# Optimization experiments

Measured on AMD Instinct MI355X. Metric: run time of the kernel, lower is better.

## Reference

```python
import jax, jax.numpy as jnp
import numpy as np

S = 7          # grid size
B = 2          # boxes per cell
C = 20         # classes
STEP = 1.0 / S
L_COORD = 5.0
L_NOOBJ = 0.5
EPS = 1e-6


def setup_inputs() -> dict:
    key = jax.random.key(0)
    k1, k2, k3 = jax.random.split(key, 3)
    N = 16384
    pred = jax.random.normal(k1, (N, S, S, B * 5 + C), dtype=jnp.float32)
    target = jax.random.uniform(k2, (N, S, S, B * 5 + C), dtype=jnp.float32)
    objm = jax.random.uniform(k3, (N, S, S, B)) < 0.05
    tb = target[..., :10].reshape(N, S, S, B, 5)
    tb = tb.at[..., 4].set(tb[..., 4] * objm)
    target = target.at[..., :10].set(tb.reshape(N, S, S, 10))
    return {"pred": pred, "target": target}


def _convert_box(box, gx, gy):
    # box: [N,S,S,B,4] in cell-relative (x,y) + image-relative (w,h)
    # gx: grid x index (axis 2), gy: grid y index (axis 1); matches conver_box
    x = (box[..., 0] + gx) * STEP - box[..., 2] * 0.5
    y = (box[..., 1] + gy) * STEP - box[..., 3] * 0.5
    out = jnp.stack([x, y, box[..., 2], box[..., 3]], axis=-1)
    return jnp.clip(out, 0.0, 1.0)


def _iou(b1, b2):
    x1, y1, w1, h1 = b1[..., 0], b1[..., 1], b1[..., 2], b1[..., 3]
    x2, y2, w2, h2 = b2[..., 0], b2[..., 1], b2[..., 2], b2[..., 3]
    inter_w = jnp.maximum(w1 + w2 - (jnp.maximum(x1 + w1, x2 + w2) - jnp.minimum(x1, x2)), 0.0)
    inter_h = jnp.maximum(h1 + h2 - (jnp.maximum(y1 + h1, y2 + h2) - jnp.minimum(y1, y2)), 0.0)
    inter = inter_w * inter_h
    union = w1 * h1 + w2 * h2 - inter + EPS
    return inter / union


def reference(pred, target):
    N = pred.shape[0]
    pb = pred[..., :10].reshape(N, S, S, B, 5)   # [N,S,S,B,5]
    tb = target[..., :10].reshape(N, S, S, B, 5)
    pc = pred[..., 10:]                           # [N,S,S,C]
    tc = target[..., 10:]
    obj0 = tb[..., 4] > 0                         # [N,S,S,B]
    sig = jnp.any(obj0, axis=-1)                  # [N,S,S]
    # grid indices: torch loop uses (y=dim1, x=dim2), conver_box index=[x, y]
    gx = jnp.arange(S, dtype=pred.dtype).reshape(1, 1, S, 1)
    gy = jnp.arange(S, dtype=pred.dtype).reshape(1, S, 1, 1)
    ious = _iou(_convert_box(pb[..., :4], gx, gy), _convert_box(tb[..., :4], gx, gy))  # [N,S,S,B]
    # responsible box = argmax IoU (first index on ties, matching torch .max(0))
    best = jnp.argmax(ious, axis=-1)[..., None] == jnp.arange(B)  # [N,S,S,B]
    obj = obj0 & best
    zero = jnp.zeros((), pred.dtype)
    # confidence losses
    dconf2 = (pb[..., 4] - tb[..., 4]) ** 2
    obj_loss = jnp.sum(jnp.where(obj, dconf2, zero))
    noobj_loss = jnp.sum(jnp.where(~obj, dconf2, zero))
    # coordinate losses
    obj_e = obj[..., None]
    dxy2 = (pb[..., :2] - tb[..., :2]) ** 2
    xy_loss = jnp.sum(jnp.where(obj_e, dxy2, zero))
    pwh = jnp.maximum(pb[..., 2:4], 0.0)
    dwh2 = (jnp.sqrt(tb[..., 2:4] + EPS) - jnp.sqrt(pwh + EPS)) ** 2
    wh_loss = jnp.sum(jnp.where(obj_e, dwh2, zero))
    # class loss over cells containing any object
    dcls2 = (pc - tc) ** 2
    class_loss = jnp.sum(jnp.where(sig[..., None], dcls2, zero))
    loss = obj_loss + L_NOOBJ * noobj_loss + L_COORD * xy_loss + L_COORD * wh_loss + class_loss
    return loss / N
```

## Files before the change

### kernel.cpp

```cpp
#include <hip/hip_runtime.h>

#define STEPV (1.0f / 7.0f)
#define L_COORD 5.0f
#define L_NOOBJ 0.5f
#define EPSV 1e-6f

#define TILE 128
#define FLOATS_PER_CELL 30
#define TILE_F4 (TILE * FLOATS_PER_CELL / 4)

typedef const __attribute__((address_space(1))) void cg_void;
typedef __attribute__((address_space(3))) void ls_void;

__global__ __launch_bounds__(384) void yolo_loss_kernel(
    const float* __restrict__ pred,
    const float* __restrict__ tgt,
    float* __restrict__ partials)
{
    __shared__ float4 bufP4[TILE_F4];
    __shared__ float4 bufT4[TILE_F4];

    const int tid  = threadIdx.x;
    const int w    = tid >> 6;
    const int lane = tid & 63;

    if (w < 3) {
        const float4* g = reinterpret_cast<const float4*>(pred)
                        + (size_t)blockIdx.x * TILE_F4 + w * 320 + lane;
        #pragma unroll
        for (int i = 0; i < 5; ++i)
            __builtin_amdgcn_global_load_lds((cg_void*)(g + i * 64),
                                             (ls_void*)(bufP4 + w * 320 + i * 64),
                                             16, 0, 0);
    } else {
        const float4* g = reinterpret_cast<const float4*>(tgt)
                        + (size_t)blockIdx.x * TILE_F4 + (w - 3) * 320 + lane;
        #pragma unroll
        for (int i = 0; i < 5; ++i)
            __builtin_amdgcn_global_load_lds((cg_void*)(g + i * 64),
                                             (ls_void*)(bufT4 + (w - 3) * 320 + i * 64),
                                             16, 0, 0);
    }
    __syncthreads();

    const float* bufP = reinterpret_cast<const float*>(bufP4);
    const float* bufT = reinterpret_cast<const float*>(bufT4);

    float loss = 0.0f;

    if (tid < TILE) {
        const int cid  = tid;
        const int cell = blockIdx.x * TILE + cid;
        const float* p = bufP + cid * FLOATS_PER_CELL;
        const float* t = bufT + cid * FLOATS_PER_CELL;
        float pv[10], tv[10];
        #pragma unroll
        for (int k = 0; k < 5; ++k) {
            float2 a = *reinterpret_cast<const float2*>(p + 2 * k);
            pv[2 * k] = a.x; pv[2 * k + 1] = a.y;
            float2 b = *reinterpret_cast<const float2*>(t + 2 * k);
            tv[2 * k] = b.x; tv[2 * k + 1] = b.y;
        }

        int ij = cell % 49;
        float gy = (float)(ij / 7);
        float gx = (float)(ij % 7);

        float iou[2];
        #pragma unroll
        for (int b = 0; b < 2; ++b) {
            const float* pb = pv + b * 5;
            const float* tb = tv + b * 5;
            float x1 = fminf(fmaxf((pb[0] + gx) * STEPV - pb[2] * 0.5f, 0.f), 1.f);
            float y1 = fminf(fmaxf((pb[1] + gy) * STEPV - pb[3] * 0.5f, 0.f), 1.f);
            float w1 = fminf(fmaxf(pb[2], 0.f), 1.f);
            float h1 = fminf(fmaxf(pb[3], 0.f), 1.f);
            float x2 = fminf(fmaxf((tb[0] + gx) * STEPV - tb[2] * 0.5f, 0.f), 1.f);
            float y2 = fminf(fmaxf((tb[1] + gy) * STEPV - tb[3] * 0.5f, 0.f), 1.f);
            float w2 = fminf(fmaxf(tb[2], 0.f), 1.f);
            float h2 = fminf(fmaxf(tb[3], 0.f), 1.f);
            float iw = fmaxf(w1 + w2 - (fmaxf(x1 + w1, x2 + w2) - fminf(x1, x2)), 0.f);
            float ih = fmaxf(h1 + h2 - (fmaxf(y1 + h1, y2 + h2) - fminf(y1, y2)), 0.f);
            float inter = iw * ih;
            float uni = w1 * h1 + w2 * h2 - inter + EPSV;
            iou[b] = inter / uni;
        }
        int best = (iou[1] > iou[0]) ? 1 : 0;

        float obj_l = 0.f, noobj_l = 0.f, xy_l = 0.f, wh_l = 0.f;
        #pragma unroll
        for (int b = 0; b < 2; ++b) {
            const float* pb = pv + b * 5;
            const float* tb = tv + b * 5;
            bool obj = (tb[4] > 0.f) && (b == best);
            float dc = pb[4] - tb[4];
            dc *= dc;
            if (obj) {
                obj_l += dc;
                float dx = pb[0] - tb[0];
                float dy = pb[1] - tb[1];
                xy_l += dx * dx + dy * dy;
                float sw = sqrtf(tb[2] + EPSV) - sqrtf(fmaxf(pb[2], 0.f) + EPSV);
                float sh = sqrtf(tb[3] + EPSV) - sqrtf(fmaxf(pb[3], 0.f) + EPSV);
                wh_l += sw * sw + sh * sh;
            } else {
                noobj_l += dc;
            }
        }
        loss = obj_l + L_NOOBJ * noobj_l + L_COORD * (xy_l + wh_l);
    } else {
        const int q   = tid - TILE;
        const int cid = q >> 1;
        const int sub = q & 1;
        const float* p = bufP + cid * FLOATS_PER_CELL + 10 + sub * 10;
        const float* t = bufT + cid * FLOATS_PER_CELL + 10 + sub * 10;
        float t4 = bufT[cid * FLOATS_PER_CELL + 4];
        float t9 = bufT[cid * FLOATS_PER_CELL + 9];
        bool sig = (t4 > 0.f) || (t9 > 0.f);

        float cls = 0.f;
        #pragma unroll
        for (int k = 0; k < 5; ++k) {
            float2 a = *reinterpret_cast<const float2*>(p + 2 * k);
            float2 b = *reinterpret_cast<const float2*>(t + 2 * k);
            float d0 = a.x - b.x;
            float d1 = a.y - b.y;
            cls += d0 * d0 + d1 * d1;
        }
        loss = sig ? cls : 0.0f;
    }

    #pragma unroll
    for (int off = 32; off > 0; off >>= 1)
        loss += __shfl_down(loss, off, 64);

    __shared__ float wsum[6];
    if (lane == 0) wsum[w] = loss;
    __syncthreads();
    if (tid == 0) {
        float s = 0.f;
        #pragma unroll
        for (int k = 0; k < 6; ++k) s += wsum[k];
        partials[blockIdx.x] = s;
    }
}

__global__ __launch_bounds__(1024) void yolo_finalize(
    const float* __restrict__ partials,
    float* __restrict__ out, int nparts, float invN)
{
    double s = 0.0;
    for (int i = threadIdx.x; i < nparts; i += 1024)
        s += (double)partials[i];

    #pragma unroll
    for (int off = 32; off > 0; off >>= 1)
        s += __shfl_down(s, off, 64);

    __shared__ double wsum[16];
    int lane = threadIdx.x & 63;
    int wid  = threadIdx.x >> 6;
    if (lane == 0) wsum[wid] = s;
    __syncthreads();
    if (threadIdx.x == 0) {
        double tot = 0.0;
        #pragma unroll
        for (int k = 0; k < 16; ++k) tot += wsum[k];
        out[0] = (float)(tot * (double)invN);
    }
}

extern "C" void kernel_launch(void* const* d_in, const int* in_sizes, int n_in,
                              void* d_out, int out_size, void* d_ws, size_t ws_size,
                              hipStream_t stream)
{
    const float* pred = (const float*)d_in[0];
    const float* tgt  = (const float*)d_in[1];
    float* out      = (float*)d_out;
    float* partials = (float*)d_ws;

    int ncells = in_sizes[0] / FLOATS_PER_CELL;
    int N = ncells / 49;
    int blocks = ncells / TILE;

    yolo_loss_kernel<<<blocks, 384, 0, stream>>>(pred, tgt, partials);
    yolo_finalize<<<1, 1024, 0, stream>>>(partials, out, blocks, 1.0f / (float)N);
}
```

Measured before the change: 36.22 us.

## Persistent grid with double-buffered async global-to-LDS tile prefetch

Replaces the one-tile-per-block launch with a fixed grid of 512 persistent blocks that stride over tiles. The next tile is prefetched into a second LDS buffer with global_load_lds while the current one is computed, using explicit vmcnt waits and barriers. The goal is to overlap memory latency with compute, cut block launch overhead, and shrink the finalize reduction to 512 partials. LDS per block doubles, which can lower occupancy, and the hand-written waitcnt ordering is fragile.

```diff
diff --git a/kernel.cpp b/kernel.cpp
--- a/kernel.cpp
+++ b/kernel.cpp
@@ -7,127 +7,147 @@
 
 #define TILE 128
 #define FLOATS_PER_CELL 30
-#define TILE_F4 (TILE * FLOATS_PER_CELL / 4)
+#define TILE_F4 960
+#define NBLK 512
+#define NTHREADS 384
 
 typedef const __attribute__((address_space(1))) void cg_void;
 typedef __attribute__((address_space(3))) void ls_void;
 
-__global__ __launch_bounds__(384) void yolo_loss_kernel(
+__global__ __launch_bounds__(NTHREADS) void yolo_loss_kernel(
     const float* __restrict__ pred,
     const float* __restrict__ tgt,
-    float* __restrict__ partials)
+    float* __restrict__ partials,
+    int ntiles)
 {
-    __shared__ float4 bufP4[TILE_F4];
-    __shared__ float4 bufT4[TILE_F4];
+    __shared__ float4 buf[2][2 * TILE_F4];
 
     const int tid  = threadIdx.x;
     const int w    = tid >> 6;
     const int lane = tid & 63;
 
-    if (w < 3) {
-        const float4* g = reinterpret_cast<const float4*>(pred)
-                        + (size_t)blockIdx.x * TILE_F4 + w * 320 + lane;
-        #pragma unroll
-        for (int i = 0; i < 5; ++i)
-            __builtin_amdgcn_global_load_lds((cg_void*)(g + i * 64),
-                                             (ls_void*)(bufP4 + w * 320 + i * 64),
-                                             16, 0, 0);
-    } else {
-        const float4* g = reinterpret_cast<const float4*>(tgt)
-                        + (size_t)blockIdx.x * TILE_F4 + (w - 3) * 320 + lane;
-        #pragma unroll
-        for (int i = 0; i < 5; ++i)
-            __builtin_amdgcn_global_load_lds((cg_void*)(g + i * 64),
-                                             (ls_void*)(bufT4 + (w - 3) * 320 + i * 64),
-                                             16, 0, 0);
-    }
-    __syncthreads();
-
-    const float* bufP = reinterpret_cast<const float*>(bufP4);
-    const float* bufT = reinterpret_cast<const float*>(bufT4);
+    const int wh   = (w < 3) ? w : (w - 3);
+    const int toff = (w < 3) ? 0 : TILE_F4;
+    const float4* gbase = reinterpret_cast<const float4*>(w < 3 ? pred : tgt);
+
+    #define STAGE(tile_, b_)                                                     \
+        do {                                                                     \
+            const float4* g_ = gbase + (size_t)(tile_) * TILE_F4 + wh * 320 + lane; \
+            float4* l_ = &buf[(b_)][toff + wh * 320];                            \
+            _Pragma("unroll")                                                    \
+            for (int i_ = 0; i_ < 5; ++i_)                                       \
+                __builtin_amdgcn_global_load_lds((cg_void*)(g_ + i_ * 64),       \
+                                                 (ls_void*)(l_ + i_ * 64),       \
+                                                 16, 0, 0);                      \
+        } while (0)
 
     float loss = 0.0f;
-
-    if (tid < TILE) {
-        const int cid  = tid;
-        const int cell = blockIdx.x * TILE + cid;
-        const float* p = bufP + cid * FLOATS_PER_CELL;
-        const float* t = bufT + cid * FLOATS_PER_CELL;
-        float pv[10], tv[10];
-        #pragma unroll
-        for (int k = 0; k < 5; ++k) {
-            float2 a = *reinterpret_cast<const float2*>(p + 2 * k);
-            pv[2 * k] = a.x; pv[2 * k + 1] = a.y;
-            float2 b = *reinterpret_cast<const float2*>(t + 2 * k);
-            tv[2 * k] = b.x; tv[2 * k + 1] = b.y;
+    int it = 0;
+
+    STAGE(blockIdx.x, 0);
+
+    for (int tile = blockIdx.x; tile < ntiles; tile += NBLK, ++it) {
+        const int b = it & 1;
+        const int nxt = tile + NBLK;
+
+        if (nxt < ntiles) {
+            STAGE(nxt, b ^ 1);
+            asm volatile("s_waitcnt vmcnt(5)" ::: "memory");
+        } else {
+            asm volatile("s_waitcnt vmcnt(0)" ::: "memory");
         }
-
-        int ij = cell % 49;
-        float gy = (float)(ij / 7);
-        float gx = (float)(ij % 7);
-
-        float iou[2];
-        #pragma unroll
-        for (int b = 0; b < 2; ++b) {
-            const float* pb = pv + b * 5;
-            const float* tb = tv + b * 5;
-            float x1 = fminf(fmaxf((pb[0] + gx) * STEPV - pb[2] * 0.5f, 0.f), 1.f);
-            float y1 = fminf(fmaxf((pb[1] + gy) * STEPV - pb[3] * 0.5f, 0.f), 1.f);
-            float w1 = fminf(fmaxf(pb[2], 0.f), 1.f);
-            float h1 = fminf(fmaxf(pb[3], 0.f), 1.f);
-            float x2 = fminf(fmaxf((tb[0] + gx) * STEPV - tb[2] * 0.5f, 0.f), 1.f);
-            float y2 = fminf(fmaxf((tb[1] + gy) * STEPV - tb[3] * 0.5f, 0.f), 1.f);
-            float w2 = fminf(fmaxf(tb[2], 0.f), 1.f);
-            float h2 = fminf(fmaxf(tb[3], 0.f), 1.f);
-            float iw = fmaxf(w1 + w2 - (fmaxf(x1 + w1, x2 + w2) - fminf(x1, x2)), 0.f);
-            float ih = fmaxf(h1 + h2 - (fmaxf(y1 + h1, y2 + h2) - fminf(y1, y2)), 0.f);
-            float inter = iw * ih;
-            float uni = w1 * h1 + w2 * h2 - inter + EPSV;
-            iou[b] = inter / uni;
+        __builtin_amdgcn_sched_barrier(0);
+        __builtin_amdgcn_s_barrier();
+        asm volatile("" ::: "memory");
+
+        const float* bufP = reinterpret_cast<const float*>(&buf[b][0]);
+        const float* bufT = reinterpret_cast<const float*>(&buf[b][TILE_F4]);
+
+        if (tid < TILE) {
+            const int cid  = tid;
+            const int cell = tile * TILE + cid;
+            const float* p = bufP + cid * FLOATS_PER_CELL;
+            const float* t = bufT + cid * FLOATS_PER_CELL;
+            float pv[10], tv[10];
+            #pragma unroll
+            for (int k = 0; k < 5; ++k) {
+                float2 a = *reinterpret_cast<const float2*>(p + 2 * k);
+                pv[2 * k] = a.x; pv[2 * k + 1] = a.y;
+                float2 c = *reinterpret_cast<const float2*>(t + 2 * k);
+                tv[2 * k] = c.x; tv[2 * k + 1] = c.y;
+            }
+
+            int ij = cell % 49;
+            float gy = (float)(ij / 7);
+            float gx = (float)(ij % 7);
+
+            float iou[2];
+            #pragma unroll
+            for (int bb = 0; bb < 2; ++bb) {
+                const float* pb = pv + bb * 5;
+                const float* tb = tv + bb * 5;
+                float x1 = fminf(fmaxf((pb[0] + gx) * STEPV - pb[2] * 0.5f, 0.f), 1.f);
+                float y1 = fminf(fmaxf((pb[1] + gy) * STEPV - pb[3] * 0.5f, 0.f), 1.f);
+                float w1 = fminf(fmaxf(pb[2], 0.f), 1.f);
+                float h1 = fminf(fmaxf(pb[3], 0.f), 1.f);
+                float x2 = fminf(fmaxf((tb[0] + gx) * STEPV - tb[2] * 0.5f, 0.f), 1.f);
+                float y2 = fminf(fmaxf((tb[1] + gy) * STEPV - tb[3] * 0.5f, 0.f), 1.f);
+                float w2 = fminf(fmaxf(tb[2], 0.f), 1.f);
+                float h2 = fminf(fmaxf(tb[3], 0.f), 1.f);
+                float iw = fmaxf(w1 + w2 - (fmaxf(x1 + w1, x2 + w2) - fminf(x1, x2)), 0.f);
+                float ih = fmaxf(h1 + h2 - (fmaxf(y1 + h1, y2 + h2) - fminf(y1, y2)), 0.f);
+                float inter = iw * ih;
+                float uni = w1 * h1 + w2 * h2 - inter + EPSV;
+                iou[bb] = inter / uni;
+            }
+            int best = (iou[1] > iou[0]) ? 1 : 0;
+
+            float obj_l = 0.f, noobj_l = 0.f, xy_l = 0.f, wh_l = 0.f;
+            #pragma unroll
+            for (int bb = 0; bb < 2; ++bb) {
+                const float* pb = pv + bb * 5;
+                const float* tb = tv + bb * 5;
+                bool obj = (tb[4] > 0.f) && (bb == best);
+                float dc = pb[4] - tb[4];
+                dc *= dc;
+                if (obj) {
+                    obj_l += dc;
+                    float dx = pb[0] - tb[0];
+                    float dy = pb[1] - tb[1];
+                    xy_l += dx * dx + dy * dy;
+                    float sw = sqrtf(tb[2] + EPSV) - sqrtf(fmaxf(pb[2], 0.f) + EPSV);
+                    float sh = sqrtf(tb[3] + EPSV) - sqrtf(fmaxf(pb[3], 0.f) + EPSV);
+                    wh_l += sw * sw + sh * sh;
+                } else {
+                    noobj_l += dc;
+                }
+            }
+            loss += obj_l + L_NOOBJ * noobj_l + L_COORD * (xy_l + wh_l);
+        } else {
+            const int q   = tid - TILE;
+            const int cid = q >> 1;
+            const int sub = q & 1;
+            const float* p = bufP + cid * FLOATS_PER_CELL + 10 + sub * 10;
+            const float* t = bufT + cid * FLOATS_PER_CELL + 10 + sub * 10;
+            float t4 = bufT[cid * FLOATS_PER_CELL + 4];
+            float t9 = bufT[cid * FLOATS_PER_CELL + 9];
+            bool sig = (t4 > 0.f) || (t9 > 0.f);
+
+            float cls = 0.f;
+            #pragma unroll
+            for (int k = 0; k < 5; ++k) {
+                float2 a = *reinterpret_cast<const float2*>(p + 2 * k);
+                float2 c = *reinterpret_cast<const float2*>(t + 2 * k);
+                float d0 = a.x - c.x;
+                float d1 = a.y - c.y;
+                cls += d0 * d0 + d1 * d1;
+            }
+            if (sig) loss += cls;
         }
-        int best = (iou[1] > iou[0]) ? 1 : 0;
-
-        float obj_l = 0.f, noobj_l = 0.f, xy_l = 0.f, wh_l = 0.f;
-        #pragma unroll
-        for (int b = 0; b < 2; ++b) {
-            const float* pb = pv + b * 5;
-            const float* tb = tv + b * 5;
-            bool obj = (tb[4] > 0.f) && (b == best);
-            float dc = pb[4] - tb[4];
-            dc *= dc;
-            if (obj) {
-                obj_l += dc;
-                float dx = pb[0] - tb[0];
-                float dy = pb[1] - tb[1];
-                xy_l += dx * dx + dy * dy;
-                float sw = sqrtf(tb[2] + EPSV) - sqrtf(fmaxf(pb[2], 0.f) + EPSV);
-                float sh = sqrtf(tb[3] + EPSV) - sqrtf(fmaxf(pb[3], 0.f) + EPSV);
-                wh_l += sw * sw + sh * sh;
-            } else {
-                noobj_l += dc;
-            }
-        }
-        loss = obj_l + L_NOOBJ * noobj_l + L_COORD * (xy_l + wh_l);
-    } else {
-        const int q   = tid - TILE;
-        const int cid = q >> 1;
-        const int sub = q & 1;
-        const float* p = bufP + cid * FLOATS_PER_CELL + 10 + sub * 10;
-        const float* t = bufT + cid * FLOATS_PER_CELL + 10 + sub * 10;
-        float t4 = bufT[cid * FLOATS_PER_CELL + 4];
-        float t9 = bufT[cid * FLOATS_PER_CELL + 9];
-        bool sig = (t4 > 0.f) || (t9 > 0.f);
-
-        float cls = 0.f;
-        #pragma unroll
-        for (int k = 0; k < 5; ++k) {
-            float2 a = *reinterpret_cast<const float2*>(p + 2 * k);
-            float2 b = *reinterpret_cast<const float2*>(t + 2 * k);
-            float d0 = a.x - b.x;
-            float d1 = a.y - b.y;
-            cls += d0 * d0 + d1 * d1;
-        }
-        loss = sig ? cls : 0.0f;
+
+        asm volatile("" ::: "memory");
+        __builtin_amdgcn_sched_barrier(0);
+        __builtin_amdgcn_s_barrier();
     }
 
     #pragma unroll
@@ -145,19 +165,19 @@
     }
 }
 
-__global__ __launch_bounds__(1024) void yolo_finalize(
+__global__ __launch_bounds__(512) void yolo_finalize(
     const float* __restrict__ partials,
     float* __restrict__ out, int nparts, float invN)
 {
     double s = 0.0;
-    for (int i = threadIdx.x; i < nparts; i += 1024)
+    for (int i = threadIdx.x; i < nparts; i += 512)
         s += (double)partials[i];
 
     #pragma unroll
     for (int off = 32; off > 0; off >>= 1)
         s += __shfl_down(s, off, 64);
 
-    __shared__ double wsum[16];
+    __shared__ double wsum[8];
     int lane = threadIdx.x & 63;
     int wid  = threadIdx.x >> 6;
     if (lane == 0) wsum[wid] = s;
@@ -165,7 +185,7 @@
     if (threadIdx.x == 0) {
         double tot = 0.0;
         #pragma unroll
-        for (int k = 0; k < 16; ++k) tot += wsum[k];
+        for (int k = 0; k < 8; ++k) tot += wsum[k];
         out[0] = (float)(tot * (double)invN);
     }
 }
@@ -181,8 +201,8 @@
 
     int ncells = in_sizes[0] / FLOATS_PER_CELL;
     int N = ncells / 49;
-    int blocks = ncells / TILE;
-
-    yolo_loss_kernel<<<blocks, 384, 0, stream>>>(pred, tgt, partials);
-    yolo_finalize<<<1, 1024, 0, stream>>>(partials, out, blocks, 1.0f / (float)N);
+    int ntiles = ncells / TILE;
+
+    yolo_loss_kernel<<<NBLK, NTHREADS, 0, stream>>>(pred, tgt, partials, ntiles);
+    yolo_finalize<<<1, 512, 0, stream>>>(partials, out, NBLK, 1.0f / (float)N);
 }
```

After: 42.12 us. 16.3% more time.
